# Optimization experiments

Hardware: AMD Instinct MI355X
Metric: run time of the kernel (lower is better)

## Reference

```python
import jax, jax.numpy as jnp
import numpy as np

B, N, DIN, DOUT, H, DH, DC, NL, L = 8, 256, 64, 64, 8, 8, 64, 32, 2
SCALE = DH ** -0.5  # out_dim-per-head scaling used by both attention variants


def _ln(x, g, b):
    m = jnp.mean(x, -1, keepdims=True)
    v = jnp.mean((x - m) ** 2, -1, keepdims=True)
    return (x - m) * jax.lax.rsqrt(v + 1e-5) * g + b


def _cross_attn(x, ctx, mask_b, wq, wkv, wo, bo):
    # CrossAttentionLayer: standard softmax attention with clamp(-5,5)
    b, n, _ = x.shape
    m = ctx.shape[1]
    q = (x @ wq).reshape(b, n, H, DH).transpose(0, 2, 1, 3)
    k, v = jnp.split(ctx @ wkv, 2, axis=-1)
    k = k.reshape(b, m, H, DH).transpose(0, 2, 1, 3)
    v = v.reshape(b, m, H, DH).transpose(0, 2, 1, 3)
    sim = jnp.einsum('bhid,bhjd->bhij', q, k) * SCALE
    if mask_b is not None:
        sim = jnp.where(mask_b[:, None, None, :], sim, -jnp.finfo(sim.dtype).max)
    sim = jnp.clip(sim, -5.0, 5.0)
    attn = jax.nn.softmax(sim, axis=-1)
    out = jnp.einsum('bhij,bhjd->bhid', attn, v)
    out = out.transpose(0, 2, 1, 3).reshape(b, n, H * DH)
    return out @ wo + bo


def _mha_edge(p, e, k_RW, mask, wq, wk, we, wv):
    # GraphiT MultiHeadAttentionLayer with edge features + k_RW attention PE
    Q = (p @ wq).reshape(B, N, H, DH)
    K = (p @ wk).reshape(B, N, H, DH) * SCALE
    V = (p @ wv).reshape(B, N, H, DH).transpose(0, 2, 1, 3)  # [B,H,N,d]
    E = (e @ we).reshape(B, N, N, H, DH)
    scores = jnp.einsum('bihk,bjhk,bijhk->bhij', Q, K, E)
    scores = jnp.exp(scores - jnp.max(scores, axis=(-2, -1), keepdims=True))
    scores = scores * mask[:, None, :, None] * mask[:, None, None, :]
    scores = scores * k_RW
    denom = jnp.clip(jnp.sum(scores, -1, keepdims=True), 1e-6, None)
    out = jnp.einsum('bhij,bhjd->bhid', scores, V) / denom
    return out.transpose(0, 2, 1, 3).reshape(B, N, H * DH)


def setup_inputs() -> dict:
    key = jax.random.key(0)
    ks = jax.random.split(key, 32)
    rn = lambda k, s: jax.random.normal(k, s, dtype=jnp.float32)
    inp = {
        'h': rn(ks[0], (B, N, DIN)),
        'p': rn(ks[1], (B, N, DIN)),
        'e': rn(ks[2], (B, N, N, DIN)),
        'k_RW': jax.random.uniform(ks[3], (B, 1, N, N), dtype=jnp.float32),
        'queries': rn(ks[4], (B, NL, DC)),
        'mask': jnp.ones((B, N), dtype=jnp.float32),
        # attention_p (MultiHeadAttentionLayer) weights
        'wq_p': rn(ks[5], (DIN, H * DH)) * 0.05,
        'wk_p': rn(ks[6], (DIN, H * DH)) * 0.05,
        'we_p': rn(ks[7], (DIN, H * DH)) * 0.05,
        'wv_p': rn(ks[8], (DIN, H * DH)) * 0.05,
        'wo_p': rn(ks[9], (DOUT, DOUT)) * 0.05,
        # cross_attention_h (queries attend to nodes)
        'cq_wq': rn(ks[10], (DC, H * DH)) * 0.05,
        'cq_wkv': rn(ks[11], (DIN, 2 * H * DH)) * 0.05,
        'cq_wo': rn(ks[12], (H * DH, DC)) * 0.05,
        'cq_bo': jnp.zeros((DC,), dtype=jnp.float32),
        # L_cross latent self-attention layers (stacked)
        'sa_wq': rn(ks[13], (L, DC, H * DH)) * 0.05,
        'sa_wkv': rn(ks[14], (L, DC, 2 * H * DH)) * 0.05,
        'sa_wo': rn(ks[15], (L, H * DH, DC)) * 0.05,
        'sa_bo': jnp.zeros((L, DC), dtype=jnp.float32),
        # O_queries, norms, FFN
        'oq_w': rn(ks[16], (DC, DC)) * 0.05,
        'ln1_g': jnp.ones((DC,), dtype=jnp.float32),
        'ln1_b': jnp.zeros((DC,), dtype=jnp.float32),
        'ffn_w1': rn(ks[17], (DC, 2 * DC)) * 0.05,
        'ffn_w2': rn(ks[18], (2 * DC, DC)) * 0.05,
        'ln2_g': jnp.ones((DC,), dtype=jnp.float32),
        'ln2_b': jnp.zeros((DC,), dtype=jnp.float32),
    }
    return inp


def reference(h, p, e, k_RW, queries, mask,
              wq_p, wk_p, we_p, wv_p, wo_p,
              cq_wq, cq_wkv, cq_wo, cq_bo,
              sa_wq, sa_wkv, sa_wo, sa_bo,
              oq_w, ln1_g, ln1_b, ffn_w1, ffn_w2, ln2_g, ln2_b):
    # forward_p: update positional encoding via edge-modulated attention
    p_attn = _mha_edge(p, e, k_RW, mask, wq_p, wk_p, we_p, wv_p)
    p_new = p + jnp.tanh(p_attn @ wo_p)  # residual, no dropout (eval)
    # combine node features with updated PE (use_node_pe='sum')
    h_c = h + p_new
    mask_b = mask > 0.5
    # perceiver cross-attention: latents attend to nodes
    q = queries + _cross_attn(queries, h_c, mask_b, cq_wq, cq_wkv, cq_wo, cq_bo)
    # L_cross latent self-attention blocks with residual
    for i in range(L):
        q = q + _cross_attn(q, q, None, sa_wq[i], sa_wkv[i], sa_wo[i], sa_bo[i])
    # O_queries projection + layer norm
    q = _ln(q @ oq_w, ln1_g, ln1_b)
    # feed-forward block on queries
    ff = jax.nn.relu(q @ ffn_w1) @ ffn_w2
    q = _ln(q + ff, ln2_g, ln2_b)
    return q
```

## Files before the change

### kernel.cpp

```cpp
#include <hip/hip_runtime.h>
#include <hip/hip_bf16.h>
#include <math.h>

typedef __bf16 bf16x8 __attribute__((ext_vector_type(8)));
typedef float floatx4 __attribute__((ext_vector_type(4)));

#define ATT_SCALE 0.35355339059327373f

__device__ __forceinline__ __bf16 f2b(float x) { return (__bf16)x; }

__global__ void k_proj(const float* __restrict__ p, const float* __restrict__ quer,
                       const float* __restrict__ wq, const float* __restrict__ wk,
                       const float* __restrict__ wv, const float* __restrict__ cq_wq,
                       float* __restrict__ Q, float* __restrict__ Ks,
                       float* __restrict__ V, float* __restrict__ q1) {
  int blk = blockIdx.x, t = threadIdx.x;
  __shared__ float xr[64];
  if (blk < 2048) {
    xr[t] = p[blk * 64 + t];
    __syncthreads();
    float aq = 0.f, ak = 0.f, av = 0.f;
    for (int c = 0; c < 64; c++) {
      float x = xr[c];
      aq += x * wq[c * 64 + t];
      ak += x * wk[c * 64 + t];
      av += x * wv[c * 64 + t];
    }
    Q[blk * 64 + t] = aq;
    Ks[blk * 64 + t] = ak * ATT_SCALE;
    V[blk * 64 + t] = av;
  } else {
    int r = blk - 2048;
    xr[t] = quer[r * 64 + t];
    __syncthreads();
    float a = 0.f;
    for (int c = 0; c < 64; c++) a += xr[c] * cq_wq[c * 64 + t];
    q1[r * 64 + t] = a;
  }
}

__global__ __launch_bounds__(256) void k_edge(
    const float* __restrict__ e, const float* __restrict__ we,
    const float* __restrict__ krw, const float* __restrict__ mask,
    const float* __restrict__ hin, const float* __restrict__ pin,
    const float* __restrict__ wo, const float* __restrict__ cq_wkv,
    const float* __restrict__ Q, const float* __restrict__ Ks,
    const float* __restrict__ V, float* __restrict__ Kc, float* __restrict__ Vc) {
  int bi = blockIdx.x;
  int b = bi >> 8;
  int t = threadIdx.x;
  int w = t >> 6, l = t & 63;
  int l15 = l & 15, quad = l >> 4, half8 = (l >> 3) & 1, d = l & 7;

  bf16x8 wfrag[4][2];
  for (int nt = 0; nt < 4; nt++)
    for (int kc = 0; kc < 2; kc++)
      for (int jj = 0; jj < 8; jj++)
        wfrag[nt][kc][jj] = f2b(we[(kc * 32 + quad * 8 + jj) * 64 + nt * 16 + l15]);

  float qv[4];
  for (int nt = 0; nt < 4; nt++) qv[nt] = Q[bi * 64 + nt * 16 + l15];
  float mi = mask[bi];

  float aout[4] = {0.f, 0.f, 0.f, 0.f};
  float aden[4] = {0.f, 0.f, 0.f, 0.f};

  for (int mt = 0; mt < 4; mt++) {
    int j0 = w * 64 + mt * 16;
    const float* ep = e + ((long)bi * 256 + j0 + l15) * 64 + quad * 8;
    float4 ea = *reinterpret_cast<const float4*>(ep);
    float4 eb4 = *reinterpret_cast<const float4*>(ep + 4);
    float4 ec = *reinterpret_cast<const float4*>(ep + 32);
    float4 ed4 = *reinterpret_cast<const float4*>(ep + 36);
    bf16x8 a0, a1;
    a0[0] = f2b(ea.x); a0[1] = f2b(ea.y); a0[2] = f2b(ea.z); a0[3] = f2b(ea.w);
    a0[4] = f2b(eb4.x); a0[5] = f2b(eb4.y); a0[6] = f2b(eb4.z); a0[7] = f2b(eb4.w);
    a1[0] = f2b(ec.x); a1[1] = f2b(ec.y); a1[2] = f2b(ec.z); a1[3] = f2b(ec.w);
    a1[4] = f2b(ed4.x); a1[5] = f2b(ed4.y); a1[6] = f2b(ed4.z); a1[7] = f2b(ed4.w);

    int jr0 = j0 + quad * 4;
    float krw_r[4], mj_r[4];
    for (int r = 0; r < 4; r++) {
      krw_r[r] = krw[(long)bi * 256 + jr0 + r];
      mj_r[r] = mask[b * 256 + jr0 + r];
    }
    for (int nt = 0; nt < 4; nt++) {
      floatx4 acc = {0.f, 0.f, 0.f, 0.f};
      acc = __builtin_amdgcn_mfma_f32_16x16x32_bf16(a0, wfrag[nt][0], acc, 0, 0, 0);
      acc = __builtin_amdgcn_mfma_f32_16x16x32_bf16(a1, wfrag[nt][1], acc, 0, 0, 0);
      int hk = nt * 16 + l15;
      int hbase = hk & 56;
      for (int r = 0; r < 4; r++) {
        int jr = jr0 + r;
        float s = acc[r] * qv[nt] * Ks[(b * 256 + jr) * 64 + hk];
        s += __shfl_xor(s, 1);
        s += __shfl_xor(s, 2);
        s += __shfl_xor(s, 4);
        float wg = __expf(s) * krw_r[r] * mj_r[r];
        aden[nt] += wg;
        aout[nt] += wg * V[(b * 256 + jr) * 64 + hbase + d];
      }
    }
  }
  for (int nt = 0; nt < 4; nt++) {
    float o = aout[nt], dn = aden[nt];
    o += __shfl_xor(o, 16); o += __shfl_xor(o, 32);
    dn += __shfl_xor(dn, 16); dn += __shfl_xor(dn, 32);
    aout[nt] = o; aden[nt] = dn;
  }

  __shared__ float red[4][64];
  __shared__ float redden[4][8];
  __shared__ float pav[64];
  __shared__ float hcl[64];
  if (l < 16) {
    for (int nt = 0; nt < 4; nt++) {
      int head = nt * 2 + half8;
      red[w][head * 8 + d] = aout[nt];
      if (d == 0) redden[w][head] = aden[nt];
    }
  }
  __syncthreads();
  if (t < 64) {
    int head = t >> 3;
    float num = red[0][t] + red[1][t] + red[2][t] + red[3][t];
    float den = redden[0][head] + redden[1][head] + redden[2][head] + redden[3][head];
    num *= mi;
    den = fmaxf(den * mi, 1e-6f);
    pav[t] = num / den;
  }
  __syncthreads();
  if (t < 64) {
    float a = 0.f;
    for (int c = 0; c < 64; c++) a += pav[c] * wo[c * 64 + t];
    hcl[t] = hin[bi * 64 + t] + pin[bi * 64 + t] + tanhf(a);
  }
  __syncthreads();
  if (t < 128) {
    float a = 0.f;
    for (int c = 0; c < 64; c++) a += hcl[c] * cq_wkv[c * 128 + t];
    if (t < 64) Kc[bi * 64 + t] = a;
    else        Vc[bi * 64 + t - 64] = a;
  }
}

__global__ void k_cross(const float* __restrict__ q1, const float* __restrict__ Kc,
                        const float* __restrict__ Vc, const float* __restrict__ mask,
                        float* __restrict__ oc) {
  int bh = blockIdx.x, b = bh >> 3, h = bh & 7;
  int t = threadIdx.x, r = t >> 3, g = t & 7;
  __shared__ float qL[32][8];
  qL[r][g] = q1[(b * 32 + r) * 64 + h * 8 + g];
  __syncthreads();
  float num[8] = {0.f, 0.f, 0.f, 0.f, 0.f, 0.f, 0.f, 0.f};
  float den = 0.f;
  for (int jj = 0; jj < 32; jj++) {
    int j = jj * 8 + g;
    const float* kp = Kc + (b * 256 + j) * 64 + h * 8;
    float s = 0.f;
    for (int dd = 0; dd < 8; dd++) s += qL[r][dd] * kp[dd];
    s *= ATT_SCALE;
    float mj = mask[b * 256 + j];
    s = (mj > 0.5f) ? s : -1e30f;
    s = fminf(fmaxf(s, -5.f), 5.f);
    float ex = __expf(s);
    den += ex;
    const float* vp = Vc + (b * 256 + j) * 64 + h * 8;
    for (int dd = 0; dd < 8; dd++) num[dd] += ex * vp[dd];
  }
  den += __shfl_xor(den, 1); den += __shfl_xor(den, 2); den += __shfl_xor(den, 4);
  for (int dd = 0; dd < 8; dd++) {
    float v = num[dd];
    v += __shfl_xor(v, 1); v += __shfl_xor(v, 2); v += __shfl_xor(v, 4);
    num[dd] = v;
  }
  oc[(b * 32 + r) * 64 + h * 8 + g] = num[g] / den;
}

__global__ void k_projqkv(const float* __restrict__ attn_in, const float* __restrict__ Wo,
                          const float* __restrict__ bo, const float* __restrict__ residp,
                          const float* __restrict__ wql, const float* __restrict__ wkvl,
                          float* __restrict__ q_out, float* __restrict__ qq,
                          float* __restrict__ kvb) {
  int r = blockIdx.x, t = threadIdx.x;
  __shared__ float oL[64];
  __shared__ float qL[64];
  oL[t] = attn_in[r * 64 + t];
  __syncthreads();
  float a = 0.f;
  for (int c = 0; c < 64; c++) a += oL[c] * Wo[c * 64 + t];
  float qvv = residp[r * 64 + t] + a + bo[t];
  q_out[r * 64 + t] = qvv;
  qL[t] = qvv;
  __syncthreads();
  float aq = 0.f, ak = 0.f, av = 0.f;
  for (int c = 0; c < 64; c++) {
    float x = qL[c];
    aq += x * wql[c * 64 + t];
    ak += x * wkvl[c * 128 + t];
    av += x * wkvl[c * 128 + 64 + t];
  }
  qq[r * 64 + t] = aq;
  kvb[r * 128 + t] = ak;
  kvb[r * 128 + 64 + t] = av;
}

__global__ void k_sattn(const float* __restrict__ qq, const float* __restrict__ kvb,
                        float* __restrict__ os) {
  int bh = blockIdx.x, b = bh >> 3, h = bh & 7;
  int t = threadIdx.x, r = t >> 3, g = t & 7;
  __shared__ float qL[32][8];
  qL[r][g] = qq[(b * 32 + r) * 64 + h * 8 + g];
  __syncthreads();
  float num[8] = {0.f, 0.f, 0.f, 0.f, 0.f, 0.f, 0.f, 0.f};
  float den = 0.f;
  for (int jj = 0; jj < 4; jj++) {
    int j = jj * 8 + g;
    const float* kp = kvb + (b * 32 + j) * 128 + h * 8;
    float s = 0.f;
    for (int dd = 0; dd < 8; dd++) s += qL[r][dd] * kp[dd];
    s *= ATT_SCALE;
    s = fminf(fmaxf(s, -5.f), 5.f);
    float ex = __expf(s);
    den += ex;
    for (int dd = 0; dd < 8; dd++) num[dd] += ex * kp[64 + dd];
  }
  den += __shfl_xor(den, 1); den += __shfl_xor(den, 2); den += __shfl_xor(den, 4);
  for (int dd = 0; dd < 8; dd++) {
    float v = num[dd];
    v += __shfl_xor(v, 1); v += __shfl_xor(v, 2); v += __shfl_xor(v, 4);
    num[dd] = v;
  }
  os[(b * 32 + r) * 64 + h * 8 + g] = num[g] / den;
}

__global__ void k_final(const float* __restrict__ os, const float* __restrict__ Wo,
                        const float* __restrict__ bo, const float* __restrict__ qprev,
                        const float* __restrict__ oqw, const float* __restrict__ g1,
                        const float* __restrict__ b1, const float* __restrict__ w1,
                        const float* __restrict__ w2, const float* __restrict__ g2,
                        const float* __restrict__ b2v, float* __restrict__ out) {
  int r = blockIdx.x, t = threadIdx.x;
  __shared__ float oL[64];
  __shared__ float q2L[64];
  __shared__ float yL[64];
  __shared__ float hhs[128];
  oL[t] = os[r * 64 + t];
  __syncthreads();
  float a = 0.f;
  for (int c = 0; c < 64; c++) a += oL[c] * Wo[c * 64 + t];
  float q2 = qprev[r * 64 + t] + a + bo[t];
  q2L[t] = q2;
  __syncthreads();
  float x = 0.f;
  for (int c = 0; c < 64; c++) x += q2L[c] * oqw[c * 64 + t];
  float m = x;
  for (int off = 1; off < 64; off <<= 1) m += __shfl_xor(m, off);
  m *= (1.f / 64.f);
  float dv = x - m, vv = dv * dv;
  for (int off = 1; off < 64; off <<= 1) vv += __shfl_xor(vv, off);
  vv *= (1.f / 64.f);
  float y = dv * rsqrtf(vv + 1e-5f) * g1[t] + b1[t];
  yL[t] = y;
  __syncthreads();
  float h1 = 0.f, h2 = 0.f;
  for (int c = 0; c < 64; c++) {
    float xx = yL[c];
    h1 += xx * w1[c * 128 + t];
    h2 += xx * w1[c * 128 + 64 + t];
  }
  hhs[t] = fmaxf(h1, 0.f);
  hhs[t + 64] = fmaxf(h2, 0.f);
  __syncthreads();
  float ff = 0.f;
  for (int c = 0; c < 128; c++) ff += hhs[c] * w2[c * 64 + t];
  float z = y + ff;
  float m2 = z;
  for (int off = 1; off < 64; off <<= 1) m2 += __shfl_xor(m2, off);
  m2 *= (1.f / 64.f);
  float dz = z - m2, v2 = dz * dz;
  for (int off = 1; off < 64; off <<= 1) v2 += __shfl_xor(v2, off);
  v2 *= (1.f / 64.f);
  float z2 = dz * rsqrtf(v2 + 1e-5f) * g2[t] + b2v[t];
  out[r * 64 + t] = z2;
}

extern "C" void kernel_launch(void* const* d_in, const int* in_sizes, int n_in,
                              void* d_out, int out_size, void* d_ws, size_t ws_size,
                              hipStream_t stream) {
  const float* h_in   = (const float*)d_in[0];
  const float* p_in   = (const float*)d_in[1];
  const float* e_in   = (const float*)d_in[2];
  const float* krw    = (const float*)d_in[3];
  const float* quer   = (const float*)d_in[4];
  const float* mask   = (const float*)d_in[5];
  const float* wq_p   = (const float*)d_in[6];
  const float* wk_p   = (const float*)d_in[7];
  const float* we_p   = (const float*)d_in[8];
  const float* wv_p   = (const float*)d_in[9];
  const float* wo_p   = (const float*)d_in[10];
  const float* cq_wq  = (const float*)d_in[11];
  const float* cq_wkv = (const float*)d_in[12];
  const float* cq_wo  = (const float*)d_in[13];
  const float* cq_bo  = (const float*)d_in[14];
  const float* sa_wq  = (const float*)d_in[15];
  const float* sa_wkv = (const float*)d_in[16];
  const float* sa_wo  = (const float*)d_in[17];
  const float* sa_bo  = (const float*)d_in[18];
  const float* oq_w   = (const float*)d_in[19];
  const float* ln1_g  = (const float*)d_in[20];
  const float* ln1_b  = (const float*)d_in[21];
  const float* ffn_w1 = (const float*)d_in[22];
  const float* ffn_w2 = (const float*)d_in[23];
  const float* ln2_g  = (const float*)d_in[24];
  const float* ln2_b  = (const float*)d_in[25];

  float* ws = (float*)d_ws;
  float* Q   = ws;
  float* Ks  = Q + 131072;
  float* V   = Ks + 131072;
  float* q1  = V + 131072;
  float* Kc  = q1 + 16384;
  float* Vc  = Kc + 131072;
  float* oc  = Vc + 131072;
  float* q0  = oc + 16384;
  float* qq  = q0 + 16384;
  float* kvb = qq + 16384;
  float* osa = kvb + 32768;
  float* qc1 = osa + 16384;

  k_proj<<<2304, 64, 0, stream>>>(p_in, quer, wq_p, wk_p, wv_p, cq_wq, Q, Ks, V, q1);
  k_edge<<<2048, 256, 0, stream>>>(e_in, we_p, krw, mask, h_in, p_in, wo_p, cq_wkv,
                                   Q, Ks, V, Kc, Vc);
  k_cross<<<64, 256, 0, stream>>>(q1, Kc, Vc, mask, oc);
  k_projqkv<<<256, 64, 0, stream>>>(oc, cq_wo, cq_bo, quer,
                                    sa_wq, sa_wkv, q0, qq, kvb);
  k_sattn<<<64, 256, 0, stream>>>(qq, kvb, osa);
  k_projqkv<<<256, 64, 0, stream>>>(osa, sa_wo, sa_bo, q0,
                                    sa_wq + 4096, sa_wkv + 8192, qc1, qq, kvb);
  k_sattn<<<64, 256, 0, stream>>>(qq, kvb, osa);
  k_final<<<256, 64, 0, stream>>>(osa, sa_wo + 4096, sa_bo + 64, qc1, oq_w,
                                  ln1_g, ln1_b, ffn_w1, ffn_w2, ln2_g, ln2_b,
                                  (float*)d_out);
}
```

Baseline: 313.3 us.

## Fuse perceiver tail into one kernel and restructure edge MFMA operand layout

Replaces the six small tail kernels (cross-attention, projections, self-attention layers, final LN/FFN) with a single per-batch 1024-thread kernel that keeps latents in shared memory, removing launch overhead and intermediate global round trips. The edge kernel swaps MFMA operand order so each lane owns one edge row, turning the per-row 3-step shuffle reduction into a single shuffle and vectorizing Ks/V loads, at the cost of 32 output accumulators per lane and a wider final reduction. The tail kernel uses only 8 blocks, so it leaves most of the GPU idle.

```diff
diff --git a/kernel.cpp b/kernel.cpp
--- a/kernel.cpp
+++ b/kernel.cpp
@@ -9,34 +9,26 @@
 
 __device__ __forceinline__ __bf16 f2b(float x) { return (__bf16)x; }
 
-__global__ void k_proj(const float* __restrict__ p, const float* __restrict__ quer,
+__global__ void k_proj(const float* __restrict__ p,
                        const float* __restrict__ wq, const float* __restrict__ wk,
-                       const float* __restrict__ wv, const float* __restrict__ cq_wq,
+                       const float* __restrict__ wv,
                        float* __restrict__ Q, float* __restrict__ Ks,
-                       float* __restrict__ V, float* __restrict__ q1) {
+                       float* __restrict__ V) {
   int blk = blockIdx.x, t = threadIdx.x;
   __shared__ float xr[64];
-  if (blk < 2048) {
-    xr[t] = p[blk * 64 + t];
-    __syncthreads();
-    float aq = 0.f, ak = 0.f, av = 0.f;
-    for (int c = 0; c < 64; c++) {
-      float x = xr[c];
-      aq += x * wq[c * 64 + t];
-      ak += x * wk[c * 64 + t];
-      av += x * wv[c * 64 + t];
-    }
-    Q[blk * 64 + t] = aq;
-    Ks[blk * 64 + t] = ak * ATT_SCALE;
-    V[blk * 64 + t] = av;
-  } else {
-    int r = blk - 2048;
-    xr[t] = quer[r * 64 + t];
-    __syncthreads();
-    float a = 0.f;
-    for (int c = 0; c < 64; c++) a += xr[c] * cq_wq[c * 64 + t];
-    q1[r * 64 + t] = a;
-  }
+  xr[t] = p[blk * 64 + t];
+  __syncthreads();
+  float aq = 0.f, ak = 0.f, av = 0.f;
+#pragma unroll 8
+  for (int c = 0; c < 64; c++) {
+    float x = xr[c];
+    aq += x * wq[c * 64 + t];
+    ak += x * wk[c * 64 + t];
+    av += x * wv[c * 64 + t];
+  }
+  Q[blk * 64 + t] = aq;
+  Ks[blk * 64 + t] = ak * ATT_SCALE;
+  V[blk * 64 + t] = av;
 }
 
 __global__ __launch_bounds__(256) void k_edge(
@@ -50,74 +42,98 @@
   int b = bi >> 8;
   int t = threadIdx.x;
   int w = t >> 6, l = t & 63;
-  int l15 = l & 15, quad = l >> 4, half8 = (l >> 3) & 1, d = l & 7;
+  int l15 = l & 15, q4 = l >> 4;
+  int head_lo = q4 >> 1;
 
   bf16x8 wfrag[4][2];
+#pragma unroll
   for (int nt = 0; nt < 4; nt++)
+#pragma unroll
     for (int kc = 0; kc < 2; kc++)
+#pragma unroll
       for (int jj = 0; jj < 8; jj++)
-        wfrag[nt][kc][jj] = f2b(we[(kc * 32 + quad * 8 + jj) * 64 + nt * 16 + l15]);
-
-  float qv[4];
-  for (int nt = 0; nt < 4; nt++) qv[nt] = Q[bi * 64 + nt * 16 + l15];
+        wfrag[nt][kc][jj] = f2b(we[(kc * 32 + q4 * 8 + jj) * 64 + nt * 16 + l15]);
+
+  float4 qv[4];
+#pragma unroll
+  for (int nt = 0; nt < 4; nt++)
+    qv[nt] = *reinterpret_cast<const float4*>(Q + bi * 64 + nt * 16 + q4 * 4);
+
   float mi = mask[bi];
 
-  float aout[4] = {0.f, 0.f, 0.f, 0.f};
-  float aden[4] = {0.f, 0.f, 0.f, 0.f};
+  float aout[4][8];
+  float aden[4];
+#pragma unroll
+  for (int nt = 0; nt < 4; nt++) {
+    aden[nt] = 0.f;
+#pragma unroll
+    for (int dd = 0; dd < 8; dd++) aout[nt][dd] = 0.f;
+  }
 
   for (int mt = 0; mt < 4; mt++) {
     int j0 = w * 64 + mt * 16;
-    const float* ep = e + ((long)bi * 256 + j0 + l15) * 64 + quad * 8;
+    int j = j0 + l15;
+    const float* ep = e + ((long)bi * 256 + j) * 64 + q4 * 8;
     float4 ea = *reinterpret_cast<const float4*>(ep);
     float4 eb4 = *reinterpret_cast<const float4*>(ep + 4);
     float4 ec = *reinterpret_cast<const float4*>(ep + 32);
     float4 ed4 = *reinterpret_cast<const float4*>(ep + 36);
-    bf16x8 a0, a1;
-    a0[0] = f2b(ea.x); a0[1] = f2b(ea.y); a0[2] = f2b(ea.z); a0[3] = f2b(ea.w);
-    a0[4] = f2b(eb4.x); a0[5] = f2b(eb4.y); a0[6] = f2b(eb4.z); a0[7] = f2b(eb4.w);
-    a1[0] = f2b(ec.x); a1[1] = f2b(ec.y); a1[2] = f2b(ec.z); a1[3] = f2b(ec.w);
-    a1[4] = f2b(ed4.x); a1[5] = f2b(ed4.y); a1[6] = f2b(ed4.z); a1[7] = f2b(ed4.w);
-
-    int jr0 = j0 + quad * 4;
-    float krw_r[4], mj_r[4];
-    for (int r = 0; r < 4; r++) {
-      krw_r[r] = krw[(long)bi * 256 + jr0 + r];
-      mj_r[r] = mask[b * 256 + jr0 + r];
-    }
+    bf16x8 b0, b1;
+    b0[0] = f2b(ea.x); b0[1] = f2b(ea.y); b0[2] = f2b(ea.z); b0[3] = f2b(ea.w);
+    b0[4] = f2b(eb4.x); b0[5] = f2b(eb4.y); b0[6] = f2b(eb4.z); b0[7] = f2b(eb4.w);
+    b1[0] = f2b(ec.x); b1[1] = f2b(ec.y); b1[2] = f2b(ec.z); b1[3] = f2b(ec.w);
+    b1[4] = f2b(ed4.x); b1[5] = f2b(ed4.y); b1[6] = f2b(ed4.z); b1[7] = f2b(ed4.w);
+
+    float wkm = krw[(long)bi * 256 + j] * mask[b * 256 + j];
+    const float* ksrow = Ks + (b * 256 + j) * 64;
+    const float* vrow = V + (b * 256 + j) * 64;
+
+#pragma unroll
     for (int nt = 0; nt < 4; nt++) {
       floatx4 acc = {0.f, 0.f, 0.f, 0.f};
-      acc = __builtin_amdgcn_mfma_f32_16x16x32_bf16(a0, wfrag[nt][0], acc, 0, 0, 0);
-      acc = __builtin_amdgcn_mfma_f32_16x16x32_bf16(a1, wfrag[nt][1], acc, 0, 0, 0);
-      int hk = nt * 16 + l15;
-      int hbase = hk & 56;
-      for (int r = 0; r < 4; r++) {
-        int jr = jr0 + r;
-        float s = acc[r] * qv[nt] * Ks[(b * 256 + jr) * 64 + hk];
-        s += __shfl_xor(s, 1);
-        s += __shfl_xor(s, 2);
-        s += __shfl_xor(s, 4);
-        float wg = __expf(s) * krw_r[r] * mj_r[r];
-        aden[nt] += wg;
-        aout[nt] += wg * V[(b * 256 + jr) * 64 + hbase + d];
-      }
-    }
-  }
+      acc = __builtin_amdgcn_mfma_f32_16x16x32_bf16(wfrag[nt][0], b0, acc, 0, 0, 0);
+      acc = __builtin_amdgcn_mfma_f32_16x16x32_bf16(wfrag[nt][1], b1, acc, 0, 0, 0);
+      float4 ks4 = *reinterpret_cast<const float4*>(ksrow + nt * 16 + q4 * 4);
+      float sp = acc[0] * qv[nt].x * ks4.x + acc[1] * qv[nt].y * ks4.y
+               + acc[2] * qv[nt].z * ks4.z + acc[3] * qv[nt].w * ks4.w;
+      float s = sp + __shfl_xor(sp, 16);
+      float wg = __expf(s) * wkm;
+      aden[nt] += wg;
+      int head = nt * 2 + head_lo;
+      float4 v0 = *reinterpret_cast<const float4*>(vrow + head * 8);
+      float4 v1 = *reinterpret_cast<const float4*>(vrow + head * 8 + 4);
+      aout[nt][0] += wg * v0.x; aout[nt][1] += wg * v0.y;
+      aout[nt][2] += wg * v0.z; aout[nt][3] += wg * v0.w;
+      aout[nt][4] += wg * v1.x; aout[nt][5] += wg * v1.y;
+      aout[nt][6] += wg * v1.z; aout[nt][7] += wg * v1.w;
+    }
+  }
+#pragma unroll
   for (int nt = 0; nt < 4; nt++) {
-    float o = aout[nt], dn = aden[nt];
-    o += __shfl_xor(o, 16); o += __shfl_xor(o, 32);
-    dn += __shfl_xor(dn, 16); dn += __shfl_xor(dn, 32);
-    aout[nt] = o; aden[nt] = dn;
+    float dn = aden[nt];
+    dn += __shfl_xor(dn, 1); dn += __shfl_xor(dn, 2);
+    dn += __shfl_xor(dn, 4); dn += __shfl_xor(dn, 8);
+    aden[nt] = dn;
+#pragma unroll
+    for (int dd = 0; dd < 8; dd++) {
+      float o = aout[nt][dd];
+      o += __shfl_xor(o, 1); o += __shfl_xor(o, 2);
+      o += __shfl_xor(o, 4); o += __shfl_xor(o, 8);
+      aout[nt][dd] = o;
+    }
   }
 
   __shared__ float red[4][64];
   __shared__ float redden[4][8];
   __shared__ float pav[64];
   __shared__ float hcl[64];
-  if (l < 16) {
+  if (l15 == 0 && (q4 & 1) == 0) {
+#pragma unroll
     for (int nt = 0; nt < 4; nt++) {
-      int head = nt * 2 + half8;
-      red[w][head * 8 + d] = aout[nt];
-      if (d == 0) redden[w][head] = aden[nt];
+      int head = nt * 2 + head_lo;
+#pragma unroll
+      for (int dd = 0; dd < 8; dd++) red[w][head * 8 + dd] = aout[nt][dd];
+      redden[w][head] = aden[nt];
     }
   }
   __syncthreads();
@@ -132,157 +148,233 @@
   __syncthreads();
   if (t < 64) {
     float a = 0.f;
+#pragma unroll 8
     for (int c = 0; c < 64; c++) a += pav[c] * wo[c * 64 + t];
     hcl[t] = hin[bi * 64 + t] + pin[bi * 64 + t] + tanhf(a);
   }
   __syncthreads();
   if (t < 128) {
     float a = 0.f;
+#pragma unroll 8
     for (int c = 0; c < 64; c++) a += hcl[c] * cq_wkv[c * 128 + t];
     if (t < 64) Kc[bi * 64 + t] = a;
     else        Vc[bi * 64 + t - 64] = a;
   }
 }
 
-__global__ void k_cross(const float* __restrict__ q1, const float* __restrict__ Kc,
-                        const float* __restrict__ Vc, const float* __restrict__ mask,
-                        float* __restrict__ oc) {
-  int bh = blockIdx.x, b = bh >> 3, h = bh & 7;
-  int t = threadIdx.x, r = t >> 3, g = t & 7;
-  __shared__ float qL[32][8];
-  qL[r][g] = q1[(b * 32 + r) * 64 + h * 8 + g];
-  __syncthreads();
-  float num[8] = {0.f, 0.f, 0.f, 0.f, 0.f, 0.f, 0.f, 0.f};
-  float den = 0.f;
-  for (int jj = 0; jj < 32; jj++) {
-    int j = jj * 8 + g;
-    const float* kp = Kc + (b * 256 + j) * 64 + h * 8;
-    float s = 0.f;
-    for (int dd = 0; dd < 8; dd++) s += qL[r][dd] * kp[dd];
-    s *= ATT_SCALE;
-    float mj = mask[b * 256 + j];
-    s = (mj > 0.5f) ? s : -1e30f;
-    s = fminf(fmaxf(s, -5.f), 5.f);
-    float ex = __expf(s);
-    den += ex;
-    const float* vp = Vc + (b * 256 + j) * 64 + h * 8;
-    for (int dd = 0; dd < 8; dd++) num[dd] += ex * vp[dd];
-  }
-  den += __shfl_xor(den, 1); den += __shfl_xor(den, 2); den += __shfl_xor(den, 4);
-  for (int dd = 0; dd < 8; dd++) {
-    float v = num[dd];
-    v += __shfl_xor(v, 1); v += __shfl_xor(v, 2); v += __shfl_xor(v, 4);
-    num[dd] = v;
-  }
-  oc[(b * 32 + r) * 64 + h * 8 + g] = num[g] / den;
-}
-
-__global__ void k_projqkv(const float* __restrict__ attn_in, const float* __restrict__ Wo,
-                          const float* __restrict__ bo, const float* __restrict__ residp,
-                          const float* __restrict__ wql, const float* __restrict__ wkvl,
-                          float* __restrict__ q_out, float* __restrict__ qq,
-                          float* __restrict__ kvb) {
-  int r = blockIdx.x, t = threadIdx.x;
-  __shared__ float oL[64];
-  __shared__ float qL[64];
-  oL[t] = attn_in[r * 64 + t];
-  __syncthreads();
-  float a = 0.f;
-  for (int c = 0; c < 64; c++) a += oL[c] * Wo[c * 64 + t];
-  float qvv = residp[r * 64 + t] + a + bo[t];
-  q_out[r * 64 + t] = qvv;
-  qL[t] = qvv;
-  __syncthreads();
-  float aq = 0.f, ak = 0.f, av = 0.f;
-  for (int c = 0; c < 64; c++) {
-    float x = qL[c];
-    aq += x * wql[c * 64 + t];
-    ak += x * wkvl[c * 128 + t];
-    av += x * wkvl[c * 128 + 64 + t];
-  }
-  qq[r * 64 + t] = aq;
-  kvb[r * 128 + t] = ak;
-  kvb[r * 128 + 64 + t] = av;
-}
-
-__global__ void k_sattn(const float* __restrict__ qq, const float* __restrict__ kvb,
-                        float* __restrict__ os) {
-  int bh = blockIdx.x, b = bh >> 3, h = bh & 7;
-  int t = threadIdx.x, r = t >> 3, g = t & 7;
-  __shared__ float qL[32][8];
-  qL[r][g] = qq[(b * 32 + r) * 64 + h * 8 + g];
-  __syncthreads();
-  float num[8] = {0.f, 0.f, 0.f, 0.f, 0.f, 0.f, 0.f, 0.f};
-  float den = 0.f;
-  for (int jj = 0; jj < 4; jj++) {
-    int j = jj * 8 + g;
-    const float* kp = kvb + (b * 32 + j) * 128 + h * 8;
-    float s = 0.f;
-    for (int dd = 0; dd < 8; dd++) s += qL[r][dd] * kp[dd];
-    s *= ATT_SCALE;
-    s = fminf(fmaxf(s, -5.f), 5.f);
-    float ex = __expf(s);
-    den += ex;
-    for (int dd = 0; dd < 8; dd++) num[dd] += ex * kp[64 + dd];
-  }
-  den += __shfl_xor(den, 1); den += __shfl_xor(den, 2); den += __shfl_xor(den, 4);
-  for (int dd = 0; dd < 8; dd++) {
-    float v = num[dd];
-    v += __shfl_xor(v, 1); v += __shfl_xor(v, 2); v += __shfl_xor(v, 4);
-    num[dd] = v;
-  }
-  os[(b * 32 + r) * 64 + h * 8 + g] = num[g] / den;
-}
-
-__global__ void k_final(const float* __restrict__ os, const float* __restrict__ Wo,
-                        const float* __restrict__ bo, const float* __restrict__ qprev,
-                        const float* __restrict__ oqw, const float* __restrict__ g1,
-                        const float* __restrict__ b1, const float* __restrict__ w1,
-                        const float* __restrict__ w2, const float* __restrict__ g2,
-                        const float* __restrict__ b2v, float* __restrict__ out) {
-  int r = blockIdx.x, t = threadIdx.x;
-  __shared__ float oL[64];
-  __shared__ float q2L[64];
-  __shared__ float yL[64];
-  __shared__ float hhs[128];
-  oL[t] = os[r * 64 + t];
-  __syncthreads();
-  float a = 0.f;
-  for (int c = 0; c < 64; c++) a += oL[c] * Wo[c * 64 + t];
-  float q2 = qprev[r * 64 + t] + a + bo[t];
-  q2L[t] = q2;
-  __syncthreads();
-  float x = 0.f;
-  for (int c = 0; c < 64; c++) x += q2L[c] * oqw[c * 64 + t];
-  float m = x;
-  for (int off = 1; off < 64; off <<= 1) m += __shfl_xor(m, off);
-  m *= (1.f / 64.f);
-  float dv = x - m, vv = dv * dv;
-  for (int off = 1; off < 64; off <<= 1) vv += __shfl_xor(vv, off);
-  vv *= (1.f / 64.f);
-  float y = dv * rsqrtf(vv + 1e-5f) * g1[t] + b1[t];
-  yL[t] = y;
-  __syncthreads();
-  float h1 = 0.f, h2 = 0.f;
-  for (int c = 0; c < 64; c++) {
-    float xx = yL[c];
-    h1 += xx * w1[c * 128 + t];
-    h2 += xx * w1[c * 128 + 64 + t];
-  }
-  hhs[t] = fmaxf(h1, 0.f);
-  hhs[t + 64] = fmaxf(h2, 0.f);
-  __syncthreads();
-  float ff = 0.f;
-  for (int c = 0; c < 128; c++) ff += hhs[c] * w2[c * 64 + t];
-  float z = y + ff;
-  float m2 = z;
-  for (int off = 1; off < 64; off <<= 1) m2 += __shfl_xor(m2, off);
-  m2 *= (1.f / 64.f);
-  float dz = z - m2, v2 = dz * dz;
-  for (int off = 1; off < 64; off <<= 1) v2 += __shfl_xor(v2, off);
-  v2 *= (1.f / 64.f);
-  float z2 = dz * rsqrtf(v2 + 1e-5f) * g2[t] + b2v[t];
-  out[r * 64 + t] = z2;
+__global__ __launch_bounds__(1024) void k_tail(
+    const float* __restrict__ quer, const float* __restrict__ Kc,
+    const float* __restrict__ Vc, const float* __restrict__ mask,
+    const float* __restrict__ cq_wq, const float* __restrict__ cq_wo,
+    const float* __restrict__ cq_bo,
+    const float* __restrict__ sa_wq, const float* __restrict__ sa_wkv,
+    const float* __restrict__ sa_wo, const float* __restrict__ sa_bo,
+    const float* __restrict__ oq_w, const float* __restrict__ g1,
+    const float* __restrict__ b1, const float* __restrict__ w1,
+    const float* __restrict__ w2, const float* __restrict__ g2,
+    const float* __restrict__ b2v, float* __restrict__ out) {
+  int b = blockIdx.x;
+  int t = threadIdx.x;
+  __shared__ float sq[32][64];
+  __shared__ float sx[32][64];
+  __shared__ float skv[32][128];
+  __shared__ float soc[32][64];
+  __shared__ float shh[32][128];
+
+  float* sqf = &sq[0][0];
+  float* sxf = &sx[0][0];
+  float* skvf = &skv[0][0];
+  float* shhf = &shh[0][0];
+
+  sqf[t] = quer[b * 2048 + t];
+  sqf[t + 1024] = quer[b * 2048 + t + 1024];
+  __syncthreads();
+
+#pragma unroll
+  for (int half = 0; half < 2; half++) {
+    int o = t + half * 1024, r = o >> 6, c = o & 63;
+    float a = 0.f;
+#pragma unroll 8
+    for (int k = 0; k < 64; k++) a += sq[r][k] * cq_wq[k * 64 + c];
+    sxf[o] = a;
+  }
+  __syncthreads();
+
+  {
+    int r = t >> 5, h = (t >> 2) & 7, s = t & 3;
+    float qv8[8];
+#pragma unroll
+    for (int dd = 0; dd < 8; dd++) qv8[dd] = sx[r][h * 8 + dd];
+    float num[8] = {0.f, 0.f, 0.f, 0.f, 0.f, 0.f, 0.f, 0.f};
+    float den = 0.f;
+    for (int jj = 0; jj < 64; jj++) {
+      int j = s * 64 + jj;
+      const float* kp = Kc + ((long)(b * 256 + j)) * 64 + h * 8;
+      float4 k0 = *reinterpret_cast<const float4*>(kp);
+      float4 k1 = *reinterpret_cast<const float4*>(kp + 4);
+      float sc = qv8[0] * k0.x + qv8[1] * k0.y + qv8[2] * k0.z + qv8[3] * k0.w
+               + qv8[4] * k1.x + qv8[5] * k1.y + qv8[6] * k1.z + qv8[7] * k1.w;
+      sc *= ATT_SCALE;
+      sc = (mask[b * 256 + j] > 0.5f) ? sc : -1e30f;
+      sc = fminf(fmaxf(sc, -5.f), 5.f);
+      float ex = __expf(sc);
+      den += ex;
+      const float* vp = Vc + ((long)(b * 256 + j)) * 64 + h * 8;
+      float4 v0 = *reinterpret_cast<const float4*>(vp);
+      float4 v1 = *reinterpret_cast<const float4*>(vp + 4);
+      num[0] += ex * v0.x; num[1] += ex * v0.y; num[2] += ex * v0.z; num[3] += ex * v0.w;
+      num[4] += ex * v1.x; num[5] += ex * v1.y; num[6] += ex * v1.z; num[7] += ex * v1.w;
+    }
+    den += __shfl_xor(den, 1); den += __shfl_xor(den, 2);
+#pragma unroll
+    for (int dd = 0; dd < 8; dd++) {
+      float v = num[dd];
+      v += __shfl_xor(v, 1); v += __shfl_xor(v, 2);
+      num[dd] = v;
+    }
+    if (s == 0) {
+      float inv = 1.f / den;
+#pragma unroll
+      for (int dd = 0; dd < 8; dd++) soc[r][h * 8 + dd] = num[dd] * inv;
+    }
+  }
+  __syncthreads();
+
+#pragma unroll
+  for (int half = 0; half < 2; half++) {
+    int o = t + half * 1024, r = o >> 6, c = o & 63;
+    float a = 0.f;
+#pragma unroll 8
+    for (int k = 0; k < 64; k++) a += soc[r][k] * cq_wo[k * 64 + c];
+    sqf[o] = sqf[o] + a + cq_bo[c];
+  }
+  __syncthreads();
+
+  for (int layer = 0; layer < 2; layer++) {
+    const float* wql = sa_wq + layer * 4096;
+    const float* wkvl = sa_wkv + layer * 8192;
+    const float* wol = sa_wo + layer * 4096;
+    const float* bol = sa_bo + layer * 64;
+
+#pragma unroll
+    for (int half = 0; half < 2; half++) {
+      int o = t + half * 1024, r = o >> 6, c = o & 63;
+      float a = 0.f;
+#pragma unroll 8
+      for (int k = 0; k < 64; k++) a += sq[r][k] * wql[k * 64 + c];
+      sxf[o] = a;
+    }
+#pragma unroll
+    for (int qu = 0; qu < 4; qu++) {
+      int o = t + qu * 1024, r = o >> 7, c = o & 127;
+      float a = 0.f;
+#pragma unroll 8
+      for (int k = 0; k < 64; k++) a += sq[r][k] * wkvl[k * 128 + c];
+      skvf[o] = a;
+    }
+    __syncthreads();
+
+    {
+      int r = t >> 5, h = (t >> 2) & 7, s = t & 3;
+      float qv8[8];
+#pragma unroll
+      for (int dd = 0; dd < 8; dd++) qv8[dd] = sx[r][h * 8 + dd];
+      float num[8] = {0.f, 0.f, 0.f, 0.f, 0.f, 0.f, 0.f, 0.f};
+      float den = 0.f;
+#pragma unroll
+      for (int jj = 0; jj < 8; jj++) {
+        int j = s * 8 + jj;
+        float sc = 0.f;
+#pragma unroll
+        for (int dd = 0; dd < 8; dd++) sc += qv8[dd] * skv[j][h * 8 + dd];
+        sc *= ATT_SCALE;
+        sc = fminf(fmaxf(sc, -5.f), 5.f);
+        float ex = __expf(sc);
+        den += ex;
+#pragma unroll
+        for (int dd = 0; dd < 8; dd++) num[dd] += ex * skv[j][64 + h * 8 + dd];
+      }
+      den += __shfl_xor(den, 1); den += __shfl_xor(den, 2);
+#pragma unroll
+      for (int dd = 0; dd < 8; dd++) {
+        float v = num[dd];
+        v += __shfl_xor(v, 1); v += __shfl_xor(v, 2);
+        num[dd] = v;
+      }
+      if (s == 0) {
+        float inv = 1.f / den;
+#pragma unroll
+        for (int dd = 0; dd < 8; dd++) soc[r][h * 8 + dd] = num[dd] * inv;
+      }
+    }
+    __syncthreads();
+
+#pragma unroll
+    for (int half = 0; half < 2; half++) {
+      int o = t + half * 1024, r = o >> 6, c = o & 63;
+      float a = 0.f;
+#pragma unroll 8
+      for (int k = 0; k < 64; k++) a += soc[r][k] * wol[k * 64 + c];
+      sqf[o] = sqf[o] + a + bol[c];
+    }
+    __syncthreads();
+  }
+
+#pragma unroll
+  for (int half = 0; half < 2; half++) {
+    int o = t + half * 1024, r = o >> 6, c = o & 63;
+    float a = 0.f;
+#pragma unroll 8
+    for (int k = 0; k < 64; k++) a += sq[r][k] * oq_w[k * 64 + c];
+    sxf[o] = a;
+  }
+  __syncthreads();
+
+  {
+    int wv = t >> 6, lc = t & 63;
+#pragma unroll
+    for (int pass = 0; pass < 2; pass++) {
+      int r = wv + pass * 16;
+      float x = sx[r][lc];
+      float m = x;
+      for (int off = 1; off < 64; off <<= 1) m += __shfl_xor(m, off);
+      m *= (1.f / 64.f);
+      float dv = x - m, vv = dv * dv;
+      for (int off = 1; off < 64; off <<= 1) vv += __shfl_xor(vv, off);
+      vv *= (1.f / 64.f);
+      sx[r][lc] = dv * rsqrtf(vv + 1e-5f) * g1[lc] + b1[lc];
+    }
+  }
+  __syncthreads();
+
+#pragma unroll
+  for (int qu = 0; qu < 4; qu++) {
+    int o = t + qu * 1024, r = o >> 7, c = o & 127;
+    float a = 0.f;
+#pragma unroll 8
+    for (int k = 0; k < 64; k++) a += sx[r][k] * w1[k * 128 + c];
+    shhf[o] = fmaxf(a, 0.f);
+  }
+  __syncthreads();
+
+  {
+    int wv = t >> 6, lc = t & 63;
+#pragma unroll
+    for (int pass = 0; pass < 2; pass++) {
+      int r = wv + pass * 16;
+      float ff = 0.f;
+#pragma unroll 8
+      for (int k = 0; k < 128; k++) ff += shh[r][k] * w2[k * 64 + lc];
+      float z = sx[r][lc] + ff;
+      float m2 = z;
+      for (int off = 1; off < 64; off <<= 1) m2 += __shfl_xor(m2, off);
+      m2 *= (1.f / 64.f);
+      float dz = z - m2, v2 = dz * dz;
+      for (int off = 1; off < 64; off <<= 1) v2 += __shfl_xor(v2, off);
+      v2 *= (1.f / 64.f);
+      out[b * 2048 + r * 64 + lc] = dz * rsqrtf(v2 + 1e-5f) * g2[lc] + b2v[lc];
+    }
+  }
 }
 
 extern "C" void kernel_launch(void* const* d_in, const int* in_sizes, int n_in,
@@ -316,30 +408,17 @@
   const float* ln2_b  = (const float*)d_in[25];
 
   float* ws = (float*)d_ws;
-  float* Q   = ws;
-  float* Ks  = Q + 131072;
-  float* V   = Ks + 131072;
-  float* q1  = V + 131072;
-  float* Kc  = q1 + 16384;
-  float* Vc  = Kc + 131072;
-  float* oc  = Vc + 131072;
-  float* q0  = oc + 16384;
-  float* qq  = q0 + 16384;
-  float* kvb = qq + 16384;
-  float* osa = kvb + 32768;
-  float* qc1 = osa + 16384;
-
-  k_proj<<<2304, 64, 0, stream>>>(p_in, quer, wq_p, wk_p, wv_p, cq_wq, Q, Ks, V, q1);
+  float* Q  = ws;
+  float* Ks = Q + 131072;
+  float* V  = Ks + 131072;
+  float* Kc = V + 131072;
+  float* Vc = Kc + 131072;
+
+  k_proj<<<2048, 64, 0, stream>>>(p_in, wq_p, wk_p, wv_p, Q, Ks, V);
   k_edge<<<2048, 256, 0, stream>>>(e_in, we_p, krw, mask, h_in, p_in, wo_p, cq_wkv,
                                    Q, Ks, V, Kc, Vc);
-  k_cross<<<64, 256, 0, stream>>>(q1, Kc, Vc, mask, oc);
-  k_projqkv<<<256, 64, 0, stream>>>(oc, cq_wo, cq_bo, quer,
-                                    sa_wq, sa_wkv, q0, qq, kvb);
-  k_sattn<<<64, 256, 0, stream>>>(qq, kvb, osa);
-  k_projqkv<<<256, 64, 0, stream>>>(osa, sa_wo, sa_bo, q0,
-                                    sa_wq + 4096, sa_wkv + 8192, qc1, qq, kvb);
-  k_sattn<<<64, 256, 0, stream>>>(qq, kvb, osa);
-  k_final<<<256, 64, 0, stream>>>(osa, sa_wo + 4096, sa_bo + 64, qc1, oq_w,
-                                  ln1_g, ln1_b, ffn_w1, ffn_w2, ln2_g, ln2_b,
-                                  (float*)d_out);
+  k_tail<<<8, 1024, 0, stream>>>(quer, Kc, Vc, mask, cq_wq, cq_wo, cq_bo,
+                                 sa_wq, sa_wkv, sa_wo, sa_bo, oq_w,
+                                 ln1_g, ln1_b, ffn_w1, ffn_w2, ln2_g, ln2_b,
+                                 (float*)d_out);
 }
```

Measured after the change: 524.4 us. 67.4% more time.
